# Kernel optimization log

Hardware: AMD Instinct MI355X
Metric: run time of the kernel (lower is better)

## Reference

```python
import jax, jax.numpy as jnp
import numpy as np

N = 50000
E = 400000


def _cheb_norm(edge_index, dtype):
    # PyG ChebConv norm (normalization='sym', lambda_max=2.0):
    # remove self loops, L_hat = -D^{-1/2} A D^{-1/2} on off-diagonal edges.
    src, dst = edge_index[0], edge_index[1]
    mask = (src != dst).astype(dtype)
    deg = jax.ops.segment_sum(mask, src, num_segments=N)
    dinv = jnp.where(deg > 0, jax.lax.rsqrt(jnp.where(deg > 0, deg, 1.0)), 0.0)
    w = -dinv[src] * dinv[dst] * mask  # [E]
    return src, dst, w


def _cheb_conv(x, src, dst, w, W0, W1, b):
    # out = T0(x) W0 + T1(x) W1 + b, T0 = x, T1 = L_hat x
    tx1 = jax.ops.segment_sum(w[:, None] * x[src], dst, num_segments=N)
    return x @ W0 + tx1 @ W1 + b


def setup_inputs() -> dict:
    key = jax.random.key(0)
    ks = jax.random.split(key, 12)
    s = 0.05
    inp = {
        "x": jax.random.normal(ks[0], (N, 128), dtype=jnp.float32),
        "edge_index": jax.random.randint(ks[1], (2, E), 0, N, dtype=jnp.int64),
        "W1_0": jax.random.normal(ks[2], (128, 256), dtype=jnp.float32) * s,
        "W1_1": jax.random.normal(ks[3], (128, 256), dtype=jnp.float32) * s,
        "b1": jnp.zeros((256,), dtype=jnp.float32),
        "W2_0": jax.random.normal(ks[4], (256, 256), dtype=jnp.float32) * s,
        "W2_1": jax.random.normal(ks[5], (256, 256), dtype=jnp.float32) * s,
        "b2": jnp.zeros((256,), dtype=jnp.float32),
        "W3_0": jax.random.normal(ks[6], (256, 256), dtype=jnp.float32) * s,
        "W3_1": jax.random.normal(ks[7], (256, 256), dtype=jnp.float32) * s,
        "b3": jnp.zeros((256,), dtype=jnp.float32),
    }
    return inp


def reference(x, edge_index, W1_0, W1_1, b1, W2_0, W2_1, b2, W3_0, W3_1, b3):
    # Eval mode: F.dropout with training=False is identity, so dropout is omitted.
    src, dst, w = _cheb_norm(edge_index, x.dtype)
    h = jax.nn.relu(_cheb_conv(x, src, dst, w, W1_0, W1_1, b1))
    h = jax.nn.relu(_cheb_conv(h, src, dst, w, W2_0, W2_1, b2))
    h = _cheb_conv(h, src, dst, w, W3_0, W3_1, b3)
    return h
```

## Files before the change

kernel.cpp:

```cpp
#include <hip/hip_runtime.h>
#include <hip/hip_bf16.h>


typedef __attribute__((ext_vector_type(8))) short bf16x8;
typedef __attribute__((ext_vector_type(4))) float f32x4;

__device__ __forceinline__ float bf2f(unsigned int lo16) {
    unsigned int t = lo16 << 16;
    return __builtin_bit_cast(float, t);
}
__device__ __forceinline__ unsigned short f2bf(float f) {
    unsigned int u = __builtin_bit_cast(unsigned int, f);
    unsigned int r = (u + 0x7fffu + ((u >> 16) & 1u)) >> 16;
    return (unsigned short)r;
}

struct PrepParams {
    const int* src;
    const int* dst;
    int* deg;
    int* cnt;
    int* rank;
    int E;
    const float* x;
    unsigned short* xb;
    int gE;
    int gC;
    const float* W[6];
    unsigned short* WT[6];
    int K[6];
};

__global__ __launch_bounds__(256) void prep_kernel(PrepParams p) {
    __shared__ float t[32][33];
    int b = blockIdx.x;
    int tid = threadIdx.x;
    if (b < p.gE) {
        int e = b * 256 + tid;
        if (e < p.E) {
            int s = p.src[e], d = p.dst[e];
            if (s != d) atomicAdd(&p.deg[s], 1);
            p.rank[e] = atomicAdd(&p.cnt[d], 1);
        }
        return;
    }
    b -= p.gE;
    if (b < p.gC) {
        long long i = (long long)b * 256 + tid;
        float4 v = reinterpret_cast<const float4*>(p.x)[i];
        ushort4 o;
        o.x = f2bf(v.x); o.y = f2bf(v.y); o.z = f2bf(v.z); o.w = f2bf(v.w);
        reinterpret_cast<ushort4*>(p.xb)[i] = o;
        return;
    }
    b -= p.gC;
    int m = b >> 6;
    int rem = b & 63;
    int K = p.K[m];
    int kb = (rem & 7) * 32, nb = (rem >> 3) * 32;
    if (kb >= K) return;
    const float* W = p.W[m];
    unsigned short* WT = p.WT[m];
    int lx = tid & 31, ly = tid >> 5;
    #pragma unroll
    for (int i = 0; i < 32; i += 8)
        t[ly + i][lx] = W[(size_t)(kb + ly + i) * 256 + nb + lx];
    __syncthreads();
    #pragma unroll
    for (int i = 0; i < 32; i += 8)
        WT[(size_t)(nb + ly + i) * K + kb + lx] = f2bf(t[lx][ly + i]);
}

__global__ __launch_bounds__(256) void scan_partial_dinv(const int* __restrict__ cnt,
                                                         int* __restrict__ part,
                                                         int* __restrict__ deg, int N) {
    __shared__ int lds[256];
    int tid = threadIdx.x;
    int base = blockIdx.x * 1024 + tid * 4;
    int s = 0;
    #pragma unroll
    for (int i = 0; i < 4; ++i) {
        if (base + i < N) {
            s += cnt[base + i];
            int d = deg[base + i];
            float dv = (d > 0) ? rsqrtf((float)d) : 0.0f;
            reinterpret_cast<float*>(deg)[base + i] = dv;
        }
    }
    lds[tid] = s;
    __syncthreads();
    for (int off = 128; off > 0; off >>= 1) {
        if (tid < off) lds[tid] += lds[tid + off];
        __syncthreads();
    }
    if (tid == 0) part[blockIdx.x] = lds[0];
}

__global__ __launch_bounds__(256) void scan_chunk(const int* __restrict__ cnt,
                                                  const int* __restrict__ part,
                                                  int* __restrict__ rowptr, int N, int NB) {
    __shared__ int lds[256];
    __shared__ int blockOff;
    int tid = threadIdx.x;
    if (tid < 64) {
        int v = (tid < NB) ? part[tid] : 0;
        int inc = v;
        #pragma unroll
        for (int off = 1; off < 64; off <<= 1) {
            int t = __shfl_up(inc, off, 64);
            if (tid >= off) inc += t;
        }
        if (tid == (int)blockIdx.x) blockOff = inc - v;
        if (blockIdx.x == 0 && tid == NB - 1) rowptr[N] = inc;
    }
    __syncthreads();
    int base = blockIdx.x * 1024 + tid * 4;
    int c[4];
    #pragma unroll
    for (int i = 0; i < 4; ++i) c[i] = (base + i < N) ? cnt[base + i] : 0;
    int ts = c[0] + c[1] + c[2] + c[3];
    lds[tid] = ts;
    __syncthreads();
    for (int off = 1; off < 256; off <<= 1) {
        int v = (tid >= off) ? lds[tid - off] : 0;
        __syncthreads();
        lds[tid] += v;
        __syncthreads();
    }
    int o = blockOff + lds[tid] - ts;
    #pragma unroll
    for (int i = 0; i < 4; ++i) {
        if (base + i < N) rowptr[base + i] = o;
        o += c[i];
    }
}

__global__ __launch_bounds__(256) void fill_kernel(const int* __restrict__ src,
                                                   const int* __restrict__ dst,
                                                   const int* __restrict__ rank,
                                                   const float* __restrict__ dinv,
                                                   const int* __restrict__ rowptr,
                                                   int2* __restrict__ epk, int E) {
    int e = blockIdx.x * blockDim.x + threadIdx.x;
    if (e < E) {
        int s = src[e], d = dst[e];
        int pos = rowptr[d] + rank[e];
        float w = (s != d) ? (-dinv[s] * dinv[d]) : 0.0f;
        epk[pos] = make_int2(s, __builtin_bit_cast(int, w));
    }
}

template <int V> struct RowT;
template <> struct RowT<4> { using T = uint2; };
template <> struct RowT<8> { using T = uint4; };

__device__ __forceinline__ void fma_row(float* acc, uint2 u, float wv) {
    acc[0] += wv * bf2f(u.x & 0xffffu);
    acc[1] += wv * bf2f(u.x >> 16);
    acc[2] += wv * bf2f(u.y & 0xffffu);
    acc[3] += wv * bf2f(u.y >> 16);
}
__device__ __forceinline__ void fma_row(float* acc, uint4 u, float wv) {
    acc[0] += wv * bf2f(u.x & 0xffffu);
    acc[1] += wv * bf2f(u.x >> 16);
    acc[2] += wv * bf2f(u.y & 0xffffu);
    acc[3] += wv * bf2f(u.y >> 16);
    acc[4] += wv * bf2f(u.z & 0xffffu);
    acc[5] += wv * bf2f(u.z >> 16);
    acc[6] += wv * bf2f(u.w & 0xffffu);
    acc[7] += wv * bf2f(u.w >> 16);
}
__device__ __forceinline__ void pack_out(unsigned short* q, const float* acc, uint2*) {
    uint2 o;
    o.x = (unsigned int)f2bf(acc[0]) | ((unsigned int)f2bf(acc[1]) << 16);
    o.y = (unsigned int)f2bf(acc[2]) | ((unsigned int)f2bf(acc[3]) << 16);
    *reinterpret_cast<uint2*>(q) = o;
}
__device__ __forceinline__ void pack_out(unsigned short* q, const float* acc, uint4*) {
    uint4 o;
    o.x = (unsigned int)f2bf(acc[0]) | ((unsigned int)f2bf(acc[1]) << 16);
    o.y = (unsigned int)f2bf(acc[2]) | ((unsigned int)f2bf(acc[3]) << 16);
    o.z = (unsigned int)f2bf(acc[4]) | ((unsigned int)f2bf(acc[5]) << 16);
    o.w = (unsigned int)f2bf(acc[6]) | ((unsigned int)f2bf(acc[7]) << 16);
    *reinterpret_cast<uint4*>(q) = o;
}

template <int F>
__global__ __launch_bounds__(256) void gather_bf16(const int* __restrict__ rowptr,
                                                   const int2* __restrict__ epk,
                                                   const unsigned short* __restrict__ xb,
                                                   unsigned short* __restrict__ txb,
                                                   int N) {
    constexpr int V = F / 32;
    using T = typename RowT<V>::T;
    int half = threadIdx.x >> 5;
    int lane = threadIdx.x & 31;
    int n = blockIdx.x * 8 + half;
    if (n >= N) return;
    int beg = rowptr[n], end = rowptr[n + 1];
    float acc[V] = {};

    int k = beg;
    for (; k + 8 <= end; k += 8) {
        int2 ep[8]; T r[8];
        #pragma unroll
        for (int j = 0; j < 8; ++j) ep[j] = epk[k + j];
        #pragma unroll
        for (int j = 0; j < 8; ++j)
            r[j] = *reinterpret_cast<const T*>(&xb[(size_t)ep[j].x * F + lane * V]);
        #pragma unroll
        for (int j = 0; j < 8; ++j)
            fma_row(acc, r[j], __builtin_bit_cast(float, ep[j].y));
    }
    for (; k + 4 <= end; k += 4) {
        int2 e0 = epk[k], e1 = epk[k + 1], e2 = epk[k + 2], e3 = epk[k + 3];
        T r0 = *reinterpret_cast<const T*>(&xb[(size_t)e0.x * F + lane * V]);
        T r1 = *reinterpret_cast<const T*>(&xb[(size_t)e1.x * F + lane * V]);
        T r2 = *reinterpret_cast<const T*>(&xb[(size_t)e2.x * F + lane * V]);
        T r3 = *reinterpret_cast<const T*>(&xb[(size_t)e3.x * F + lane * V]);
        fma_row(acc, r0, __builtin_bit_cast(float, e0.y));
        fma_row(acc, r1, __builtin_bit_cast(float, e1.y));
        fma_row(acc, r2, __builtin_bit_cast(float, e2.y));
        fma_row(acc, r3, __builtin_bit_cast(float, e3.y));
    }
    for (; k < end; ++k) {
        int2 e = epk[k];
        T r = *reinterpret_cast<const T*>(&xb[(size_t)e.x * F + lane * V]);
        fma_row(acc, r, __builtin_bit_cast(float, e.y));
    }

    pack_out(&txb[(size_t)n * F + lane * V], acc, (T*)nullptr);
}

template <int K, bool RELU, typename OutT>
__global__ __launch_bounds__(256, 2) void gemm_mfma(const unsigned short* __restrict__ Xb,
                                                    const unsigned short* __restrict__ Tb,
                                                    const unsigned short* __restrict__ W0T,
                                                    const unsigned short* __restrict__ W1T,
                                                    const float* __restrict__ bias,
                                                    OutT* __restrict__ out, int M) {
    __shared__ unsigned short As[128 * 64];
    __shared__ unsigned short Bs[256 * 64];

    const int tid = threadIdx.x;
    const int wave = tid >> 6;
    const int lane = tid & 63;
    const int l15 = lane & 15;
    const int quad = lane >> 4;
    const int row0 = blockIdx.x * 128;
    const int swz = ((lane & 7) ^ ((lane >> 3) & 7)) * 8;

    f32x4 acc[8][4];
    #pragma unroll
    for (int i = 0; i < 8; ++i)
        #pragma unroll
        for (int j = 0; j < 4; ++j) acc[i][j] = (f32x4){0.f, 0.f, 0.f, 0.f};

    typedef const __attribute__((address_space(1))) void gvoid;
    typedef __attribute__((address_space(3))) void lvoid;

    #pragma unroll
    for (int pass = 0; pass < 2; ++pass) {
        const unsigned short* Amat = pass ? Tb : Xb;
        const unsigned short* Wmat = pass ? W1T : W0T;
        for (int k0 = 0; k0 < K; k0 += 64) {
            if (pass != 0 || k0 != 0) __syncthreads();
            #pragma unroll
            for (int r = 0; r < 4; ++r) {
                int grow = row0 + r * 32 + wave * 8 + (lane >> 3);
                if (grow > M - 1) grow = M - 1;
                const unsigned short* gp = &Amat[(size_t)grow * K + k0 + swz];
                __builtin_amdgcn_global_load_lds((gvoid*)gp,
                    (lvoid*)&As[(r * 32 + wave * 8) * 64], 16, 0, 0);
            }
            #pragma unroll
            for (int r = 0; r < 8; ++r) {
                int brow = r * 32 + wave * 8 + (lane >> 3);
                const unsigned short* gp = &Wmat[(size_t)brow * K + k0 + swz];
                __builtin_amdgcn_global_load_lds((gvoid*)gp,
                    (lvoid*)&Bs[(r * 32 + wave * 8) * 64], 16, 0, 0);
            }
            __syncthreads();

            #pragma unroll
            for (int kf = 0; kf < 2; ++kf) {
                const int col = (((kf * 4 + quad) ^ (l15 & 7)) * 8);
                bf16x8 b[4];
                #pragma unroll
                for (int nt = 0; nt < 4; ++nt)
                    b[nt] = *reinterpret_cast<const bf16x8*>(
                        &Bs[(wave * 64 + nt * 16 + l15) * 64 + col]);
                #pragma unroll
                for (int mt = 0; mt < 8; ++mt) {
                    bf16x8 a = *reinterpret_cast<const bf16x8*>(
                        &As[(mt * 16 + l15) * 64 + col]);
                    #pragma unroll
                    for (int nt = 0; nt < 4; ++nt)
                        acc[mt][nt] = __builtin_amdgcn_mfma_f32_16x16x32_bf16(
                            a, b[nt], acc[mt][nt], 0, 0, 0);
                }
            }
        }
    }

    #pragma unroll
    for (int mt = 0; mt < 8; ++mt) {
        #pragma unroll
        for (int r = 0; r < 4; ++r) {
            int m = row0 + mt * 16 + quad * 4 + r;
            if (m >= M) continue;
            #pragma unroll
            for (int nt = 0; nt < 4; ++nt) {
                int n = wave * 64 + nt * 16 + l15;
                float v = acc[mt][nt][r] + bias[n];
                if (RELU) v = fmaxf(v, 0.0f);
                if constexpr (sizeof(OutT) == 2)
                    out[(size_t)m * 256 + n] = (OutT)f2bf(v);
                else
                    out[(size_t)m * 256 + n] = (OutT)v;
            }
        }
    }
}

static inline size_t align_up(size_t v, size_t a) { return (v + a - 1) / a * a; }

extern "C" void kernel_launch(void* const* d_in, const int* in_sizes, int n_in,
                              void* d_out, int out_size, void* d_ws, size_t ws_size,
                              hipStream_t stream) {
    const float* x    = (const float*)d_in[0];
    const int*   ei   = (const int*)d_in[1];
    const float* W1_0 = (const float*)d_in[2];
    const float* W1_1 = (const float*)d_in[3];
    const float* b1   = (const float*)d_in[4];
    const float* W2_0 = (const float*)d_in[5];
    const float* W2_1 = (const float*)d_in[6];
    const float* b2   = (const float*)d_in[7];
    const float* W3_0 = (const float*)d_in[8];
    const float* W3_1 = (const float*)d_in[9];
    const float* b3   = (const float*)d_in[10];
    float* out = (float*)d_out;

    const int N = in_sizes[0] / 128;
    const int E = in_sizes[1] / 2;
    const int* src = ei;
    const int* dst = ei + E;

    typedef unsigned short u16;
    char* ws = (char*)d_ws;
    size_t off = 0;
    int*   deg    = (int*)  (ws + off); off = align_up(off + (size_t)N * 4, 256);
    int*   cnt    = (int*)  (ws + off); off = align_up(off + (size_t)N * 4, 256);
    size_t zero_end = off;
    int*   rank   = (int*)  (ws + off); off = align_up(off + (size_t)E * 4, 256);
    int*   rowptr = (int*)  (ws + off); off = align_up(off + (size_t)(N + 1) * 4, 256);
    int*   part   = (int*)  (ws + off); off = align_up(off + 256 * 4, 256);
    int2*  epk    = (int2*) (ws + off); off = align_up(off + (size_t)E * 8, 256);
    u16*   xb     = (u16*)  (ws + off); off = align_up(off + (size_t)N * 128 * 2, 256);
    u16*   txb    = (u16*)  (ws + off); off = align_up(off + (size_t)N * 256 * 2, 256);
    u16*   h1b    = (u16*)  (ws + off); off = align_up(off + (size_t)N * 256 * 2, 256);
    u16*   h2b    = (u16*)  (ws + off); off = align_up(off + (size_t)N * 256 * 2, 256);
    u16*   W10T   = (u16*)  (ws + off); off = align_up(off + (size_t)256 * 128 * 2, 256);
    u16*   W11T   = (u16*)  (ws + off); off = align_up(off + (size_t)256 * 128 * 2, 256);
    u16*   W20T   = (u16*)  (ws + off); off = align_up(off + (size_t)256 * 256 * 2, 256);
    u16*   W21T   = (u16*)  (ws + off); off = align_up(off + (size_t)256 * 256 * 2, 256);
    u16*   W30T   = (u16*)  (ws + off); off = align_up(off + (size_t)256 * 256 * 2, 256);
    u16*   W31T   = (u16*)  (ws + off); off = align_up(off + (size_t)256 * 256 * 2, 256);
    (void)ws_size;

    const int TB = 256;
    const int gE = (E + TB - 1) / TB;
    const int gC = (int)(((long long)N * 128 / 4) / 256);
    const int NB = (N + 1023) / 1024;

    hipMemsetAsync(deg, 0, zero_end, stream);

    {
        PrepParams p;
        p.src = src; p.dst = dst; p.deg = deg; p.cnt = cnt; p.rank = rank; p.E = E;
        p.x = x; p.xb = xb; p.gE = gE; p.gC = gC;
        p.W[0] = W1_0; p.WT[0] = W10T; p.K[0] = 128;
        p.W[1] = W1_1; p.WT[1] = W11T; p.K[1] = 128;
        p.W[2] = W2_0; p.WT[2] = W20T; p.K[2] = 256;
        p.W[3] = W2_1; p.WT[3] = W21T; p.K[3] = 256;
        p.W[4] = W3_0; p.WT[4] = W30T; p.K[4] = 256;
        p.W[5] = W3_1; p.WT[5] = W31T; p.K[5] = 256;
        prep_kernel<<<gE + gC + 384, TB, 0, stream>>>(p);
    }

    scan_partial_dinv<<<NB, 256, 0, stream>>>(cnt, part, deg, N);
    scan_chunk<<<NB, 256, 0, stream>>>(cnt, part, rowptr, N, NB);
    fill_kernel<<<(E + TB - 1) / TB, TB, 0, stream>>>(src, dst, rank,
                                                      (const float*)deg, rowptr, epk, E);

    dim3 gemmGrid((N + 127) / 128);
    dim3 gatherGrid((N + 7) / 8);

    gather_bf16<128><<<gatherGrid, TB, 0, stream>>>(rowptr, epk, xb, txb, N);
    gemm_mfma<128, true, u16><<<gemmGrid, TB, 0, stream>>>(xb, txb, W10T, W11T, b1, h1b, N);

    gather_bf16<256><<<gatherGrid, TB, 0, stream>>>(rowptr, epk, h1b, txb, N);
    gemm_mfma<256, true, u16><<<gemmGrid, TB, 0, stream>>>(h1b, txb, W20T, W21T, b2, h2b, N);

    gather_bf16<256><<<gatherGrid, TB, 0, stream>>>(rowptr, epk, h2b, txb, N);
    gemm_mfma<256, false, float><<<gemmGrid, TB, 0, stream>>>(h2b, txb, W30T, W31T, b3, out, N);
}
```

Baseline: 309.0 us.

## Double-buffer GEMM LDS tiles and split output columns across two blocks

The fused two-pass MFMA GEMM now runs a double-buffered pipeline: the next K-step's A/B tiles are prefetched into alternate LDS buffers while the current step computes, with explicit vmcnt waits and barriers. The output is also split into two 128-column halves via a second grid dimension, which halves per-block accumulators and B tile size and doubles the block count for better occupancy. In exchange, each A tile is loaded twice (once per column half), and the hand-written waitcnt/barrier sequencing is fragile.

```diff
diff --git a/kernel.cpp b/kernel.cpp
--- a/kernel.cpp
+++ b/kernel.cpp
@@ -239,8 +239,10 @@
                                                     const unsigned short* __restrict__ W1T,
                                                     const float* __restrict__ bias,
                                                     OutT* __restrict__ out, int M) {
-    __shared__ unsigned short As[128 * 64];
-    __shared__ unsigned short Bs[256 * 64];
+    constexpr int KSTEPS = K / 64;
+    constexpr int NT = 2 * KSTEPS;
+    __shared__ unsigned short As[2][128 * 64];
+    __shared__ unsigned short Bs[2][128 * 64];
 
     const int tid = threadIdx.x;
     const int wave = tid >> 6;
@@ -248,59 +250,76 @@
     const int l15 = lane & 15;
     const int quad = lane >> 4;
     const int row0 = blockIdx.x * 128;
+    const int col0 = blockIdx.y * 128;
     const int swz = ((lane & 7) ^ ((lane >> 3) & 7)) * 8;
 
-    f32x4 acc[8][4];
+    f32x4 acc[8][2];
     #pragma unroll
     for (int i = 0; i < 8; ++i)
         #pragma unroll
-        for (int j = 0; j < 4; ++j) acc[i][j] = (f32x4){0.f, 0.f, 0.f, 0.f};
+        for (int j = 0; j < 2; ++j) acc[i][j] = (f32x4){0.f, 0.f, 0.f, 0.f};
 
     typedef const __attribute__((address_space(1))) void gvoid;
     typedef __attribute__((address_space(3))) void lvoid;
 
-    #pragma unroll
-    for (int pass = 0; pass < 2; ++pass) {
-        const unsigned short* Amat = pass ? Tb : Xb;
-        const unsigned short* Wmat = pass ? W1T : W0T;
-        for (int k0 = 0; k0 < K; k0 += 64) {
-            if (pass != 0 || k0 != 0) __syncthreads();
+    auto stage = [&](int t, int buf) {
+        const unsigned short* Amat = (t < KSTEPS) ? Xb : Tb;
+        const unsigned short* Wmat = (t < KSTEPS) ? W0T : W1T;
+        const int k0 = (t & (KSTEPS - 1)) * 64;
+        #pragma unroll
+        for (int r = 0; r < 4; ++r) {
+            int grow = row0 + r * 32 + wave * 8 + (lane >> 3);
+            if (grow > M - 1) grow = M - 1;
+            const unsigned short* gp = &Amat[(size_t)grow * K + k0 + swz];
+            __builtin_amdgcn_global_load_lds((gvoid*)gp,
+                (lvoid*)&As[buf][(r * 32 + wave * 8) * 64], 16, 0, 0);
+        }
+        #pragma unroll
+        for (int r = 0; r < 4; ++r) {
+            int brow = col0 + r * 32 + wave * 8 + (lane >> 3);
+            const unsigned short* gp = &Wmat[(size_t)brow * K + k0 + swz];
+            __builtin_amdgcn_global_load_lds((gvoid*)gp,
+                (lvoid*)&Bs[buf][(r * 32 + wave * 8) * 64], 16, 0, 0);
+        }
+    };
+
+    stage(0, 0);
+    asm volatile("s_waitcnt vmcnt(0)" ::: "memory");
+    __builtin_amdgcn_s_barrier();
+
+    int cur = 0;
+    for (int t = 0; t < NT; ++t) {
+        if (t + 1 < NT) {
+            stage(t + 1, cur ^ 1);
+            asm volatile("s_waitcnt vmcnt(8)" ::: "memory");
+        } else {
+            asm volatile("s_waitcnt vmcnt(0)" ::: "memory");
+        }
+        __builtin_amdgcn_s_barrier();
+        __builtin_amdgcn_sched_barrier(0);
+
+        #pragma unroll
+        for (int kf = 0; kf < 2; ++kf) {
+            const int col = (((kf * 4 + quad) ^ (l15 & 7)) * 8);
+            bf16x8 b[2];
             #pragma unroll
-            for (int r = 0; r < 4; ++r) {
-                int grow = row0 + r * 32 + wave * 8 + (lane >> 3);
-                if (grow > M - 1) grow = M - 1;
-                const unsigned short* gp = &Amat[(size_t)grow * K + k0 + swz];
-                __builtin_amdgcn_global_load_lds((gvoid*)gp,
-                    (lvoid*)&As[(r * 32 + wave * 8) * 64], 16, 0, 0);
+            for (int nt = 0; nt < 2; ++nt)
+                b[nt] = *reinterpret_cast<const bf16x8*>(
+                    &Bs[cur][(wave * 32 + nt * 16 + l15) * 64 + col]);
+            #pragma unroll
+            for (int mt = 0; mt < 8; ++mt) {
+                bf16x8 a = *reinterpret_cast<const bf16x8*>(
+                    &As[cur][(mt * 16 + l15) * 64 + col]);
+                #pragma unroll
+                for (int nt = 0; nt < 2; ++nt)
+                    acc[mt][nt] = __builtin_amdgcn_mfma_f32_16x16x32_bf16(
+                        a, b[nt], acc[mt][nt], 0, 0, 0);
             }
-            #pragma unroll
-            for (int r = 0; r < 8; ++r) {
-                int brow = r * 32 + wave * 8 + (lane >> 3);
-                const unsigned short* gp = &Wmat[(size_t)brow * K + k0 + swz];
-                __builtin_amdgcn_global_load_lds((gvoid*)gp,
-                    (lvoid*)&Bs[(r * 32 + wave * 8) * 64], 16, 0, 0);
-            }
-            __syncthreads();
-
-            #pragma unroll
-            for (int kf = 0; kf < 2; ++kf) {
-                const int col = (((kf * 4 + quad) ^ (l15 & 7)) * 8);
-                bf16x8 b[4];
-                #pragma unroll
-                for (int nt = 0; nt < 4; ++nt)
-                    b[nt] = *reinterpret_cast<const bf16x8*>(
-                        &Bs[(wave * 64 + nt * 16 + l15) * 64 + col]);
-                #pragma unroll
-                for (int mt = 0; mt < 8; ++mt) {
-                    bf16x8 a = *reinterpret_cast<const bf16x8*>(
-                        &As[(mt * 16 + l15) * 64 + col]);
-                    #pragma unroll
-                    for (int nt = 0; nt < 4; ++nt)
-                        acc[mt][nt] = __builtin_amdgcn_mfma_f32_16x16x32_bf16(
-                            a, b[nt], acc[mt][nt], 0, 0, 0);
-                }
-            }
-        }
+        }
+
+        __builtin_amdgcn_sched_barrier(0);
+        __builtin_amdgcn_s_barrier();
+        cur ^= 1;
     }
 
     #pragma unroll
@@ -310,8 +329,8 @@
             int m = row0 + mt * 16 + quad * 4 + r;
             if (m >= M) continue;
             #pragma unroll
-            for (int nt = 0; nt < 4; ++nt) {
-                int n = wave * 64 + nt * 16 + l15;
+            for (int nt = 0; nt < 2; ++nt) {
+                int n = col0 + wave * 32 + nt * 16 + l15;
                 float v = acc[mt][nt][r] + bias[n];
                 if (RELU) v = fmaxf(v, 0.0f);
                 if constexpr (sizeof(OutT) == 2)
@@ -393,7 +412,7 @@
     fill_kernel<<<(E + TB - 1) / TB, TB, 0, stream>>>(src, dst, rank,
                                                       (const float*)deg, rowptr, epk, E);
 
-    dim3 gemmGrid((N + 127) / 128);
+    dim3 gemmGrid((N + 127) / 128, 2);
     dim3 gatherGrid((N + 7) / 8);
 
     gather_bf16<128><<<gatherGrid, TB, 0, stream>>>(rowptr, epk, xb, txb, N);
```

Measured after the change: 332.2 us. +7.5%, slower.
